# Performance work log

Measured on AMD Instinct MI355X. Metric: run time of the kernel, lower is better.

Reference implementation:

```python
import jax, jax.numpy as jnp
import numpy as np

N_NODES = 50000
N_EDGES = 800000
IN_CH = 64
HID = 128
OUT_AGE, OUT_SEX, OUT_ETH = 21, 2, 5


def _glorot(key, shape):
    fan_in, fan_out = shape
    lim = float(np.sqrt(6.0 / (fan_in + fan_out)))
    return jax.random.uniform(key, shape, jnp.float32, -lim, lim)


def sage_conv(x, src, dst, Wl, Wr, b, n_nodes):
    # PyG SAGEConv (mean aggr): out = lin_l(mean_{j->i} x_j) + lin_r(x_i) + bias
    msg_sum = jax.ops.segment_sum(x[src], dst, num_segments=n_nodes)  # [N, d]
    deg = jax.ops.segment_sum(jnp.ones((src.shape[0],), x.dtype), dst,
                              num_segments=n_nodes)  # [N]
    mean = msg_sum / jnp.maximum(deg, 1.0)[:, None]
    return mean @ Wl + x @ Wr + b


def setup_inputs() -> dict:
    key = jax.random.key(0)
    ks = jax.random.split(key, 16)
    x = jax.random.normal(ks[0], (N_NODES, IN_CH), jnp.float32)
    edge_src = jax.random.randint(ks[1], (N_EDGES,), 0, N_NODES)
    edge_dst = jax.random.randint(ks[2], (N_EDGES,), 0, N_NODES)
    dims = [(IN_CH, HID), (HID, HID), (HID, HID),
            (HID, OUT_AGE), (HID, OUT_SEX), (HID, OUT_ETH)]
    names = ['1', '2', '3', 'age', 'sex', 'eth']
    inp = {'x': x, 'edge_src': edge_src, 'edge_dst': edge_dst}
    for i, (nm, (di, do)) in enumerate(zip(names, dims)):
        inp[f'Wl_{nm}'] = _glorot(ks[3 + 2 * i], (di, do))
        inp[f'Wr_{nm}'] = _glorot(ks[4 + 2 * i], (di, do))
        inp[f'b_{nm}'] = jnp.zeros((do,), jnp.float32)
    return inp


def reference(x, edge_src, edge_dst,
              Wl_1, Wr_1, b_1, Wl_2, Wr_2, b_2, Wl_3, Wr_3, b_3,
              Wl_age, Wr_age, b_age, Wl_sex, Wr_sex, b_sex,
              Wl_eth, Wr_eth, b_eth):
    n = x.shape[0]
    h = jax.nn.relu(sage_conv(x, edge_src, edge_dst, Wl_1, Wr_1, b_1, n))
    h = jax.nn.relu(sage_conv(h, edge_src, edge_dst, Wl_2, Wr_2, b_2, n))
    h = jax.nn.relu(sage_conv(h, edge_src, edge_dst, Wl_3, Wr_3, b_3, n))
    age = sage_conv(h, edge_src, edge_dst, Wl_age, Wr_age, b_age, n)
    sex = sage_conv(h, edge_src, edge_dst, Wl_sex, Wr_sex, b_sex, n)
    eth = sage_conv(h, edge_src, edge_dst, Wl_eth, Wr_eth, b_eth, n)
    return (age, sex, eth)
```

## Files before the change

### kernel.cpp

```cpp
#include <hip/hip_runtime.h>
#include <hip/hip_bf16.h>


typedef __attribute__((ext_vector_type(8))) short bf16x8;
typedef __attribute__((ext_vector_type(4))) float f32x4;

#define NBSH 7
#define EPW  4096

__device__ __forceinline__ unsigned short f2b(float f) {
    __hip_bfloat16 h = __float2bfloat16(f);
    return *reinterpret_cast<unsigned short*>(&h);
}
__device__ __forceinline__ float b2f(unsigned short u) {
    __hip_bfloat16 h;
    *reinterpret_cast<unsigned short*>(&h) = u;
    return __bfloat162float(h);
}

__global__ void bucket_hist(const int* __restrict__ dst, int* __restrict__ ghist,
                            int n_edges, int nb) {
    __shared__ int lh[512];
    int tid = threadIdx.x;
    for (int i = tid; i < 512; i += 256) lh[i] = 0;
    __syncthreads();
    int stride = gridDim.x * blockDim.x;
    for (int e = blockIdx.x * blockDim.x + tid; e < n_edges; e += stride)
        atomicAdd(&lh[dst[e] >> NBSH], 1);
    __syncthreads();
    for (int i = tid; i < nb; i += 256)
        if (lh[i]) atomicAdd(&ghist[i], lh[i]);
}

__global__ void scan_buckets(const int* __restrict__ hist, int* __restrict__ base,
                             int* __restrict__ cur, int nb, int n_edges) {
    __shared__ int tmp[512];
    int t = threadIdx.x;
    int v = (t < nb) ? hist[t] : 0;
    tmp[t] = v;
    __syncthreads();
    for (int off = 1; off < 512; off <<= 1) {
        int u = (t >= off) ? tmp[t - off] : 0;
        __syncthreads();
        tmp[t] += u;
        __syncthreads();
    }
    if (t < nb) {
        base[t] = tmp[t] - v;
        cur[t] = tmp[t] - v;
    }
    if (t == 0) base[nb] = n_edges;
}

__global__ __launch_bounds__(512) void bin_edges_lds(
    const int* __restrict__ src, const int* __restrict__ dst,
    int* __restrict__ bkt_cur, uint2* __restrict__ ebuf, int n_edges, int nb) {
    __shared__ int hist[512];
    __shared__ int hbase[513];
    __shared__ int hcur[512];
    __shared__ uint2 sorted[EPW];
    int tid = threadIdx.x;
    int chunk0 = blockIdx.x * EPW;
    int cnt = min(EPW, n_edges - chunk0);
    hist[tid] = 0;
    __syncthreads();
    for (int i = tid; i < cnt; i += 512) atomicAdd(&hist[dst[chunk0 + i] >> NBSH], 1);
    __syncthreads();
    int v = hist[tid];
    hbase[tid] = v;
    __syncthreads();
    for (int off = 1; off < 512; off <<= 1) {
        int u = (tid >= off) ? hbase[tid - off] : 0;
        __syncthreads();
        hbase[tid] += u;
        __syncthreads();
    }
    int excl = hbase[tid] - v;
    __syncthreads();
    hbase[tid] = excl;
    hcur[tid] = excl;
    if (tid == 511) hbase[512] = excl + v;
    __syncthreads();
    for (int i = tid; i < cnt; i += 512) {
        int s = src[chunk0 + i];
        int d = dst[chunk0 + i];
        int p = atomicAdd(&hcur[d >> NBSH], 1);
        sorted[p] = make_uint2((unsigned)s, (unsigned)d);
    }
    __syncthreads();
    int cntb = hbase[tid + 1] - hbase[tid];
    int gb = 0;
    if (tid < nb && cntb > 0) gb = atomicAdd(&bkt_cur[tid], cntb);
    hist[tid] = gb;
    __syncthreads();
    for (int i = tid; i < cnt; i += 512) {
        uint2 ed = sorted[i];
        int b = (int)(ed.y >> NBSH);
        ebuf[hist[b] + (i - hbase[b])] = ed;
    }
}

__global__ void bucket_degi(const uint2* __restrict__ ebuf, const int* __restrict__ bkt_base,
                            int* __restrict__ degi, int n_nodes) {
    __shared__ int ld[128];
    int b = blockIdx.x, tid = threadIdx.x;
    int lo = b << NBSH;
    if (tid < 128) ld[tid] = 0;
    __syncthreads();
    int s = bkt_base[b], t = bkt_base[b + 1];
    for (int i = s + tid; i < t; i += 256) atomicAdd(&ld[(int)ebuf[i].y - lo], 1);
    __syncthreads();
    int hi = min(lo + 128, n_nodes);
    if (tid < hi - lo) degi[lo + tid] = ld[tid];
}

__global__ void scan_local(const int* __restrict__ degi, int* __restrict__ loc,
                           int* __restrict__ bsum, int n) {
    __shared__ int tmp[256];
    int i = blockIdx.x * 256 + threadIdx.x;
    int v = (i < n) ? degi[i] : 0;
    tmp[threadIdx.x] = v;
    __syncthreads();
    for (int off = 1; off < 256; off <<= 1) {
        int t = (threadIdx.x >= off) ? tmp[threadIdx.x - off] : 0;
        __syncthreads();
        tmp[threadIdx.x] += t;
        __syncthreads();
    }
    if (i < n) loc[i] = tmp[threadIdx.x] - v;
    if (threadIdx.x == 255) bsum[blockIdx.x] = tmp[255];
}

__global__ void scan_block(int* __restrict__ bsum, int nblk) {
    __shared__ int tmp[256];
    int v = (threadIdx.x < nblk) ? bsum[threadIdx.x] : 0;
    tmp[threadIdx.x] = v;
    __syncthreads();
    for (int off = 1; off < 256; off <<= 1) {
        int t = (threadIdx.x >= off) ? tmp[threadIdx.x - off] : 0;
        __syncthreads();
        tmp[threadIdx.x] += t;
        __syncthreads();
    }
    if (threadIdx.x < nblk) bsum[threadIdx.x] = tmp[threadIdx.x] - v;
}

__global__ void scan_add(const int* __restrict__ loc, const int* __restrict__ bsum,
                         int* __restrict__ row_start, int n, int n_edges) {
    int i = blockIdx.x * 256 + threadIdx.x;
    if (i < n) row_start[i] = loc[i] + bsum[blockIdx.x];
    if (i == 0) row_start[n] = n_edges;
}

__global__ void scatter2(const uint2* __restrict__ ebuf, const int* __restrict__ bkt_base,
                         const int* __restrict__ row_start, int* __restrict__ col,
                         int n_nodes) {
    __shared__ int lcur[128];
    int b = blockIdx.x, tid = threadIdx.x;
    int lo = b << NBSH;
    int hi = min(lo + 128, n_nodes);
    if (tid < hi - lo) lcur[tid] = row_start[lo + tid];
    __syncthreads();
    int s = bkt_base[b], t = bkt_base[b + 1];
    for (int i = s + tid; i < t; i += 256) {
        uint2 ed = ebuf[i];
        int p = atomicAdd(&lcur[(int)ed.y - lo], 1);
        col[p] = (int)ed.x;
    }
}

__global__ void convert_x(const float* __restrict__ x, unsigned short* __restrict__ xb,
                          int n4) {
    int t = blockIdx.x * blockDim.x + threadIdx.x;
    if (t >= n4) return;
    float4 v = reinterpret_cast<const float4*>(x)[t];
    uint2 o;
    o.x = (unsigned)f2b(v.x) | ((unsigned)f2b(v.y) << 16);
    o.y = (unsigned)f2b(v.z) | ((unsigned)f2b(v.w) << 16);
    reinterpret_cast<uint2*>(xb)[t] = o;
}

__global__ void build_bt(const float* __restrict__ Wl, const float* __restrict__ Wr,
                         unsigned short* __restrict__ Bt, int KA) {
    int KTOT = 2 * KA;
    int idx = blockIdx.x * blockDim.x + threadIdx.x;
    if (idx >= 128 * KTOT) return;
    int n = idx / KTOT, k = idx % KTOT;
    float v = (k < KA) ? Wl[k * 128 + n] : Wr[(k - KA) * 128 + n];
    Bt[idx] = f2b(v);
}

__global__ void cat_kernel(const float* __restrict__ Wl_age, const float* __restrict__ Wl_sex,
                           const float* __restrict__ Wl_eth, const float* __restrict__ Wr_age,
                           const float* __restrict__ Wr_sex, const float* __restrict__ Wr_eth,
                           const float* __restrict__ b_age, const float* __restrict__ b_sex,
                           const float* __restrict__ b_eth, float* __restrict__ Wl_cat,
                           float* __restrict__ Wr_cat, float* __restrict__ b_cat) {
    int idx = blockIdx.x * blockDim.x + threadIdx.x;
    if (idx < 128 * 28) {
        int k = idx / 28, j = idx % 28;
        float vl, vr;
        if (j < 21) {
            vl = Wl_age[k * 21 + j];
            vr = Wr_age[k * 21 + j];
        } else if (j < 23) {
            vl = Wl_sex[k * 2 + (j - 21)];
            vr = Wr_sex[k * 2 + (j - 21)];
        } else {
            vl = Wl_eth[k * 5 + (j - 23)];
            vr = Wr_eth[k * 5 + (j - 23)];
        }
        Wl_cat[idx] = vl;
        Wr_cat[idx] = vr;
    }
    if (idx < 28) {
        b_cat[idx] = (idx < 21) ? b_age[idx] : (idx < 23) ? b_sex[idx - 21] : b_eth[idx - 23];
    }
}

__global__ void agg128_bf(const unsigned short* __restrict__ feat,
                          const int* __restrict__ row_start, const int* __restrict__ col,
                          unsigned short* __restrict__ mean, int n_nodes) {
    int wave = (blockIdx.x * blockDim.x + threadIdx.x) >> 6;
    int lane = threadIdx.x & 63;
    if (wave >= n_nodes) return;
    int s0 = row_start[wave];
    int deg = row_start[wave + 1] - s0;
    const unsigned* f2 = reinterpret_cast<const unsigned*>(feat);
    float a0 = 0.f, a1 = 0.f, b0 = 0.f, b1 = 0.f;
    float c0 = 0.f, c1 = 0.f, d0 = 0.f, d1 = 0.f;
    for (int base = 0; base < deg; base += 64) {
        int blk = min(64, deg - base);
        int cv = col[s0 + base + min(lane, blk - 1)];
        int i = 0;
        for (; i + 3 < blk; i += 4) {
            int e0 = __shfl(cv, i), e1 = __shfl(cv, i + 1);
            int e2 = __shfl(cv, i + 2), e3 = __shfl(cv, i + 3);
            unsigned u0 = f2[(size_t)e0 * 64 + lane];
            unsigned u1 = f2[(size_t)e1 * 64 + lane];
            unsigned u2 = f2[(size_t)e2 * 64 + lane];
            unsigned u3 = f2[(size_t)e3 * 64 + lane];
            a0 += b2f((unsigned short)(u0 & 0xffff)); a1 += b2f((unsigned short)(u0 >> 16));
            b0 += b2f((unsigned short)(u1 & 0xffff)); b1 += b2f((unsigned short)(u1 >> 16));
            c0 += b2f((unsigned short)(u2 & 0xffff)); c1 += b2f((unsigned short)(u2 >> 16));
            d0 += b2f((unsigned short)(u3 & 0xffff)); d1 += b2f((unsigned short)(u3 >> 16));
        }
        for (; i < blk; ++i) {
            int e0 = __shfl(cv, i);
            unsigned u0 = f2[(size_t)e0 * 64 + lane];
            a0 += b2f((unsigned short)(u0 & 0xffff)); a1 += b2f((unsigned short)(u0 >> 16));
        }
    }
    float inv = (deg > 0) ? 1.0f / (float)deg : 0.0f;
    float sA = (a0 + b0) + (c0 + d0);
    float sB = (a1 + b1) + (c1 + d1);
    unsigned o = (unsigned)f2b(sA * inv) | ((unsigned)f2b(sB * inv) << 16);
    reinterpret_cast<unsigned*>(mean)[(size_t)wave * 64 + lane] = o;
}

__global__ void agg64_bf(const unsigned short* __restrict__ feat,
                         const int* __restrict__ row_start, const int* __restrict__ col,
                         unsigned short* __restrict__ mean, int n_nodes) {
    int wave = (blockIdx.x * blockDim.x + threadIdx.x) >> 6;
    int lane = threadIdx.x & 63;
    if (wave >= n_nodes) return;
    int sub = lane >> 5;
    int lp = lane & 31;
    int s0 = row_start[wave];
    int s1 = row_start[wave + 1];
    const unsigned* f2 = reinterpret_cast<const unsigned*>(feat);
    float a0 = 0.f, a1 = 0.f;
    for (int e = s0 + sub; e < s1; e += 2) {
        unsigned u = f2[(size_t)col[e] * 32 + lp];
        a0 += b2f((unsigned short)(u & 0xffff));
        a1 += b2f((unsigned short)(u >> 16));
    }
    a0 += __shfl_down(a0, 32);
    a1 += __shfl_down(a1, 32);
    if (sub == 0) {
        int deg = s1 - s0;
        float inv = (deg > 0) ? 1.0f / (float)deg : 0.0f;
        unsigned o = (unsigned)f2b(a0 * inv) | ((unsigned)f2b(a1 * inv) << 16);
        reinterpret_cast<unsigned*>(mean)[(size_t)wave * 32 + lp] = o;
    }
}

template <int KTOT, int KA>
__global__ __launch_bounds__(256) void mfma_layer(
    const unsigned short* __restrict__ A0, const unsigned short* __restrict__ A1,
    const unsigned short* __restrict__ Bt, const float* __restrict__ bias,
    unsigned short* __restrict__ out, int n_nodes) {
    constexpr int KC = KTOT / 64;
    __shared__ __align__(16) unsigned short sA[64][72];
    __shared__ __align__(16) unsigned short sB[128][72];
    int node0 = blockIdx.x * 64;
    int tid = threadIdx.x;
    int w = tid >> 6, lane = tid & 63;
    f32x4 acc[8] = {};
    for (int kc = 0; kc < KC; ++kc) {
        const unsigned short* Asrc;
        int kbase, aw;
        if (kc * 64 < KA) { Asrc = A0; kbase = kc * 64; aw = KA; }
        else              { Asrc = A1; kbase = kc * 64 - KA; aw = KTOT - KA; }
        {
            int nd = tid >> 2, k16 = (tid & 3) * 16;
            uint4 v0 = {0, 0, 0, 0}, v1 = {0, 0, 0, 0};
            int gn = node0 + nd;
            if (gn < n_nodes) {
                const uint4* src = reinterpret_cast<const uint4*>(Asrc + (size_t)gn * aw + kbase + k16);
                v0 = src[0];
                v1 = src[1];
            }
            uint4* dst = reinterpret_cast<uint4*>(&sA[nd][k16]);
            dst[0] = v0;
            dst[1] = v1;
        }
        {
            int n = tid >> 1, k32 = (tid & 1) * 32;
            const uint4* src = reinterpret_cast<const uint4*>(Bt + (size_t)n * KTOT + kc * 64 + k32);
            uint4* dst = reinterpret_cast<uint4*>(&sB[n][k32]);
            dst[0] = src[0];
            dst[1] = src[1];
            dst[2] = src[2];
            dst[3] = src[3];
        }
        __syncthreads();
#pragma unroll
        for (int ks = 0; ks < 2; ++ks) {
            int kl = ks * 32 + (lane >> 4) * 8;
            bf16x8 af = *reinterpret_cast<const bf16x8*>(&sA[w * 16 + (lane & 15)][kl]);
#pragma unroll
            for (int t = 0; t < 8; ++t) {
                bf16x8 bfr = *reinterpret_cast<const bf16x8*>(&sB[t * 16 + (lane & 15)][kl]);
                acc[t] = __builtin_amdgcn_mfma_f32_16x16x32_bf16(af, bfr, acc[t], 0, 0, 0);
            }
        }
        __syncthreads();
    }
    int r0 = w * 16, cq = lane >> 4, cr = lane & 15;
#pragma unroll
    for (int t = 0; t < 8; ++t) {
        int colj = t * 16 + cr;
        float bv = bias[colj];
#pragma unroll
        for (int i = 0; i < 4; ++i) {
            int node = node0 + r0 + cq * 4 + i;
            if (node < n_nodes) {
                float v = fmaxf(acc[t][i] + bv, 0.0f);
                out[(size_t)node * 128 + colj] = f2b(v);
            }
        }
    }
}

__global__ void proj_kernel(const unsigned short* __restrict__ h,
                            const float* __restrict__ Wl_cat, float* __restrict__ p,
                            int n_nodes) {
    const int NPB = 4;
    int node0 = blockIdx.x * NPB;
    __shared__ float sh[NPB][128];
    for (int idx = threadIdx.x; idx < NPB * 128; idx += blockDim.x) {
        int n = idx >> 7, k = idx & 127;
        int node = node0 + n;
        if (node < n_nodes) sh[n][k] = b2f(h[(size_t)node * 128 + k]);
    }
    __syncthreads();
    int n = threadIdx.x >> 5, j = threadIdx.x & 31;
    int node = node0 + n;
    if (node >= n_nodes) return;
    float acc = 0.f;
    if (j < 28)
        for (int k = 0; k < 128; k++) acc += sh[n][k] * Wl_cat[k * 28 + j];
    p[(size_t)node * 32 + j] = acc;
}

__global__ void agg_gather32(const float* __restrict__ p, const int* __restrict__ row_start,
                             const int* __restrict__ col, float* __restrict__ meanp,
                             int n_nodes) {
    int gid = blockIdx.x * blockDim.x + threadIdx.x;
    int node = gid >> 5;
    int j = gid & 31;
    if (node >= n_nodes) return;
    int s0 = row_start[node];
    int s1 = row_start[node + 1];
    float a = 0.f, b = 0.f;
    int e = s0;
    for (; e + 1 < s1; e += 2) {
        a += p[(size_t)col[e] * 32 + j];
        b += p[(size_t)col[e + 1] * 32 + j];
    }
    if (e < s1) a += p[(size_t)col[e] * 32 + j];
    int deg = s1 - s0;
    float inv = (deg > 0) ? 1.0f / (float)deg : 0.0f;
    meanp[(size_t)node * 32 + j] = (a + b) * inv;
}

__global__ void head_out_kernel(const unsigned short* __restrict__ h,
                                const float* __restrict__ meanp,
                                const float* __restrict__ Wr_cat, const float* __restrict__ b_cat,
                                float* __restrict__ age, float* __restrict__ sex,
                                float* __restrict__ eth, int n_nodes) {
    const int NPB = 4;
    int node0 = blockIdx.x * NPB;
    __shared__ float sh[NPB][128];
    for (int idx = threadIdx.x; idx < NPB * 128; idx += blockDim.x) {
        int n = idx >> 7, k = idx & 127;
        int node = node0 + n;
        if (node < n_nodes) sh[n][k] = b2f(h[(size_t)node * 128 + k]);
    }
    __syncthreads();
    int n = threadIdx.x >> 5, j = threadIdx.x & 31;
    int node = node0 + n;
    if (node >= n_nodes || j >= 28) return;
    float acc = b_cat[j] + meanp[(size_t)node * 32 + j];
    for (int k = 0; k < 128; k++) acc += sh[n][k] * Wr_cat[k * 28 + j];
    if (j < 21)
        age[(size_t)node * 21 + j] = acc;
    else if (j < 23)
        sex[(size_t)node * 2 + (j - 21)] = acc;
    else
        eth[(size_t)node * 5 + (j - 23)] = acc;
}

extern "C" void kernel_launch(void* const* d_in, const int* in_sizes, int n_in,
                              void* d_out, int out_size, void* d_ws, size_t ws_size,
                              hipStream_t stream) {
    const float* x        = (const float*)d_in[0];
    const int*   edge_src = (const int*)d_in[1];
    const int*   edge_dst = (const int*)d_in[2];
    const float* Wl_1 = (const float*)d_in[3];
    const float* Wr_1 = (const float*)d_in[4];
    const float* b_1  = (const float*)d_in[5];
    const float* Wl_2 = (const float*)d_in[6];
    const float* Wr_2 = (const float*)d_in[7];
    const float* b_2  = (const float*)d_in[8];
    const float* Wl_3 = (const float*)d_in[9];
    const float* Wr_3 = (const float*)d_in[10];
    const float* b_3  = (const float*)d_in[11];
    const float* Wl_age = (const float*)d_in[12];
    const float* Wr_age = (const float*)d_in[13];
    const float* b_age  = (const float*)d_in[14];
    const float* Wl_sex = (const float*)d_in[15];
    const float* Wr_sex = (const float*)d_in[16];
    const float* b_sex  = (const float*)d_in[17];
    const float* Wl_eth = (const float*)d_in[18];
    const float* Wr_eth = (const float*)d_in[19];
    const float* b_eth  = (const float*)d_in[20];

    const int n_nodes = in_sizes[0] / 64;
    const int n_edges = in_sizes[1];

    char* ws = (char*)d_ws;
    int*            degi      = (int*)(ws + 0);
    int*            row_start = (int*)(ws + 200192);
    int*            col       = (int*)(ws + 600576);
    unsigned short* Bt1       = (unsigned short*)(ws + 3800832);
    unsigned short* Bt2       = (unsigned short*)(ws + 3833600);
    unsigned short* Bt3       = (unsigned short*)(ws + 3899136);
    float*          Wl_cat    = (float*)(ws + 3964672);
    float*          Wr_cat    = (float*)(ws + 3979008);
    float*          b_cat     = (float*)(ws + 3993344);
    unsigned short* xb        = (unsigned short*)(ws + 3993600);
    unsigned short* h_bf      = (unsigned short*)(ws + 10393856);
    unsigned short* mean_bf   = (unsigned short*)(ws + 23194112);
    float*          p         = (float*)(ws + 35994368);
    float*          meanp     = (float*)(ws + 42394624);
    int*            scan_loc  = (int*)(ws + 48794880);
    int*            scan_bsum = (int*)(ws + 48995072);
    uint2*          ebuf      = (uint2*)p;
    int*            bkt_hist  = (int*)meanp;
    int*            bkt_base  = bkt_hist + 512;
    int*            bkt_cur   = bkt_hist + 1032;

    float* out_age = (float*)d_out;
    float* out_sex = out_age + (size_t)n_nodes * 21;
    float* out_eth = out_sex + (size_t)n_nodes * 2;

    const int nb        = (n_nodes + 127) >> NBSH;
    const int nchunks   = (n_edges + EPW - 1) / EPW;
    const int nblk_scan = (n_nodes + 255) / 256;

    hipMemsetAsync(bkt_hist, 0, 512 * sizeof(int), stream);
    bucket_hist<<<256, 256, 0, stream>>>(edge_dst, bkt_hist, n_edges, nb);
    scan_buckets<<<1, 512, 0, stream>>>(bkt_hist, bkt_base, bkt_cur, nb, n_edges);
    bin_edges_lds<<<nchunks, 512, 0, stream>>>(edge_src, edge_dst, bkt_cur, ebuf, n_edges, nb);
    bucket_degi<<<nb, 256, 0, stream>>>(ebuf, bkt_base, degi, n_nodes);
    scan_local<<<nblk_scan, 256, 0, stream>>>(degi, scan_loc, scan_bsum, n_nodes);
    scan_block<<<1, 256, 0, stream>>>(scan_bsum, nblk_scan);
    scan_add<<<nblk_scan, 256, 0, stream>>>(scan_loc, scan_bsum, row_start, n_nodes, n_edges);
    scatter2<<<nb, 256, 0, stream>>>(ebuf, bkt_base, row_start, col, n_nodes);

    convert_x<<<(n_nodes * 64 / 4 + 255) / 256, 256, 0, stream>>>(x, xb, n_nodes * 64 / 4);
    build_bt<<<(128 * 128 + 255) / 256, 256, 0, stream>>>(Wl_1, Wr_1, Bt1, 64);
    build_bt<<<(128 * 256 + 255) / 256, 256, 0, stream>>>(Wl_2, Wr_2, Bt2, 128);
    build_bt<<<(128 * 256 + 255) / 256, 256, 0, stream>>>(Wl_3, Wr_3, Bt3, 128);
    cat_kernel<<<(128 * 28 + 255) / 256, 256, 0, stream>>>(
        Wl_age, Wl_sex, Wl_eth, Wr_age, Wr_sex, Wr_eth, b_age, b_sex, b_eth,
        Wl_cat, Wr_cat, b_cat);

    const int agg_grid  = (n_nodes * 64 + 255) / 256;
    const int gemm_grid = (n_nodes + 63) / 64;

    agg64_bf<<<agg_grid, 256, 0, stream>>>(xb, row_start, col, mean_bf, n_nodes);
    mfma_layer<128, 64><<<gemm_grid, 256, 0, stream>>>(mean_bf, xb, Bt1, b_1, h_bf, n_nodes);

    agg128_bf<<<agg_grid, 256, 0, stream>>>(h_bf, row_start, col, mean_bf, n_nodes);
    mfma_layer<256, 128><<<gemm_grid, 256, 0, stream>>>(mean_bf, h_bf, Bt2, b_2, h_bf, n_nodes);

    agg128_bf<<<agg_grid, 256, 0, stream>>>(h_bf, row_start, col, mean_bf, n_nodes);
    mfma_layer<256, 128><<<gemm_grid, 256, 0, stream>>>(mean_bf, h_bf, Bt3, b_3, h_bf, n_nodes);

    proj_kernel<<<(n_nodes + 3) / 4, 128, 0, stream>>>(h_bf, Wl_cat, p, n_nodes);
    agg_gather32<<<(n_nodes * 32 + 255) / 256, 256, 0, stream>>>(p, row_start, col, meanp, n_nodes);
    head_out_kernel<<<(n_nodes + 3) / 4, 128, 0, stream>>>(
        h_bf, meanp, Wr_cat, b_cat, out_age, out_sex, out_eth, n_nodes);
}
```

Measured before the change: 391.1 us.

## Fuse prep kernels and batch neighbor index loads in 64/32-wide gathers

Merges the x conversion, the three weight-transpose kernels and the head-weight concatenation into one prep_all launch, removing four kernel launches. agg64_bf and agg_gather32 now load a block of column indices cooperatively, broadcast them with shuffles, and keep four independent accumulators, so more feature loads are in flight at once. The costs are extra shuffle instructions and more registers per thread.

```diff
diff --git a/kernel.cpp b/kernel.cpp
--- a/kernel.cpp
+++ b/kernel.cpp
@@ -169,52 +169,72 @@
     }
 }
 
-__global__ void convert_x(const float* __restrict__ x, unsigned short* __restrict__ xb,
-                          int n4) {
-    int t = blockIdx.x * blockDim.x + threadIdx.x;
-    if (t >= n4) return;
-    float4 v = reinterpret_cast<const float4*>(x)[t];
-    uint2 o;
-    o.x = (unsigned)f2b(v.x) | ((unsigned)f2b(v.y) << 16);
-    o.y = (unsigned)f2b(v.z) | ((unsigned)f2b(v.w) << 16);
-    reinterpret_cast<uint2*>(xb)[t] = o;
-}
-
-__global__ void build_bt(const float* __restrict__ Wl, const float* __restrict__ Wr,
-                         unsigned short* __restrict__ Bt, int KA) {
+__device__ __forceinline__ void bt_body(const float* __restrict__ Wl,
+                                        const float* __restrict__ Wr,
+                                        unsigned short* __restrict__ Bt,
+                                        int KA, int idx) {
     int KTOT = 2 * KA;
-    int idx = blockIdx.x * blockDim.x + threadIdx.x;
     if (idx >= 128 * KTOT) return;
     int n = idx / KTOT, k = idx % KTOT;
     float v = (k < KA) ? Wl[k * 128 + n] : Wr[(k - KA) * 128 + n];
     Bt[idx] = f2b(v);
 }
 
-__global__ void cat_kernel(const float* __restrict__ Wl_age, const float* __restrict__ Wl_sex,
-                           const float* __restrict__ Wl_eth, const float* __restrict__ Wr_age,
-                           const float* __restrict__ Wr_sex, const float* __restrict__ Wr_eth,
-                           const float* __restrict__ b_age, const float* __restrict__ b_sex,
-                           const float* __restrict__ b_eth, float* __restrict__ Wl_cat,
-                           float* __restrict__ Wr_cat, float* __restrict__ b_cat) {
-    int idx = blockIdx.x * blockDim.x + threadIdx.x;
-    if (idx < 128 * 28) {
-        int k = idx / 28, j = idx % 28;
-        float vl, vr;
-        if (j < 21) {
-            vl = Wl_age[k * 21 + j];
-            vr = Wr_age[k * 21 + j];
-        } else if (j < 23) {
-            vl = Wl_sex[k * 2 + (j - 21)];
-            vr = Wr_sex[k * 2 + (j - 21)];
-        } else {
-            vl = Wl_eth[k * 5 + (j - 23)];
-            vr = Wr_eth[k * 5 + (j - 23)];
-        }
-        Wl_cat[idx] = vl;
-        Wr_cat[idx] = vr;
-    }
-    if (idx < 28) {
-        b_cat[idx] = (idx < 21) ? b_age[idx] : (idx < 23) ? b_sex[idx - 21] : b_eth[idx - 23];
+__global__ void prep_all(const float* __restrict__ x, unsigned short* __restrict__ xb, int n4,
+                         const float* __restrict__ Wl1, const float* __restrict__ Wr1,
+                         unsigned short* __restrict__ Bt1,
+                         const float* __restrict__ Wl2, const float* __restrict__ Wr2,
+                         unsigned short* __restrict__ Bt2,
+                         const float* __restrict__ Wl3, const float* __restrict__ Wr3,
+                         unsigned short* __restrict__ Bt3,
+                         const float* __restrict__ Wl_age, const float* __restrict__ Wl_sex,
+                         const float* __restrict__ Wl_eth,
+                         const float* __restrict__ Wr_age, const float* __restrict__ Wr_sex,
+                         const float* __restrict__ Wr_eth,
+                         const float* __restrict__ b_age, const float* __restrict__ b_sex,
+                         const float* __restrict__ b_eth,
+                         float* __restrict__ Wl_cat, float* __restrict__ Wr_cat,
+                         float* __restrict__ b_cat) {
+    int nbx = (n4 + 255) / 256;
+    int b = blockIdx.x;
+    if (b < nbx) {
+        int t = b * 256 + threadIdx.x;
+        if (t < n4) {
+            float4 v = reinterpret_cast<const float4*>(x)[t];
+            uint2 o;
+            o.x = (unsigned)f2b(v.x) | ((unsigned)f2b(v.y) << 16);
+            o.y = (unsigned)f2b(v.z) | ((unsigned)f2b(v.w) << 16);
+            reinterpret_cast<uint2*>(xb)[t] = o;
+        }
+        return;
+    }
+    b -= nbx;
+    if (b < 64)  { bt_body(Wl1, Wr1, Bt1, 64,  b * 256 + threadIdx.x); return; }
+    b -= 64;
+    if (b < 128) { bt_body(Wl2, Wr2, Bt2, 128, b * 256 + threadIdx.x); return; }
+    b -= 128;
+    if (b < 128) { bt_body(Wl3, Wr3, Bt3, 128, b * 256 + threadIdx.x); return; }
+    b -= 128;
+    {
+        int idx = b * 256 + threadIdx.x;
+        if (idx < 128 * 28) {
+            int k = idx / 28, j = idx % 28;
+            float vl, vr;
+            if (j < 21) {
+                vl = Wl_age[k * 21 + j];
+                vr = Wr_age[k * 21 + j];
+            } else if (j < 23) {
+                vl = Wl_sex[k * 2 + (j - 21)];
+                vr = Wr_sex[k * 2 + (j - 21)];
+            } else {
+                vl = Wl_eth[k * 5 + (j - 23)];
+                vr = Wr_eth[k * 5 + (j - 23)];
+            }
+            Wl_cat[idx] = vl;
+            Wr_cat[idx] = vr;
+        }
+        if (idx < 28)
+            b_cat[idx] = (idx < 21) ? b_age[idx] : (idx < 23) ? b_sex[idx - 21] : b_eth[idx - 23];
     }
 }
 
@@ -264,23 +284,44 @@
     int wave = (blockIdx.x * blockDim.x + threadIdx.x) >> 6;
     int lane = threadIdx.x & 63;
     if (wave >= n_nodes) return;
-    int sub = lane >> 5;
+    int half = lane >> 5;
     int lp = lane & 31;
     int s0 = row_start[wave];
-    int s1 = row_start[wave + 1];
+    int deg = row_start[wave + 1] - s0;
     const unsigned* f2 = reinterpret_cast<const unsigned*>(feat);
-    float a0 = 0.f, a1 = 0.f;
-    for (int e = s0 + sub; e < s1; e += 2) {
-        unsigned u = f2[(size_t)col[e] * 32 + lp];
-        a0 += b2f((unsigned short)(u & 0xffff));
-        a1 += b2f((unsigned short)(u >> 16));
-    }
-    a0 += __shfl_down(a0, 32);
-    a1 += __shfl_down(a1, 32);
-    if (sub == 0) {
-        int deg = s1 - s0;
+    float a0 = 0.f, a1 = 0.f, b0 = 0.f, b1 = 0.f;
+    float c0 = 0.f, c1 = 0.f, d0 = 0.f, d1 = 0.f;
+    for (int base = 0; base < deg; base += 64) {
+        int blk = min(64, deg - base);
+        int cv = col[s0 + base + min(lane, blk - 1)];
+        int nfull = blk & ~7;
+        for (int i = half * 4; i < nfull; i += 8) {
+            int e0 = __shfl(cv, i), e1 = __shfl(cv, i + 1);
+            int e2 = __shfl(cv, i + 2), e3 = __shfl(cv, i + 3);
+            unsigned u0 = f2[(size_t)e0 * 32 + lp];
+            unsigned u1 = f2[(size_t)e1 * 32 + lp];
+            unsigned u2 = f2[(size_t)e2 * 32 + lp];
+            unsigned u3 = f2[(size_t)e3 * 32 + lp];
+            a0 += b2f((unsigned short)(u0 & 0xffff)); a1 += b2f((unsigned short)(u0 >> 16));
+            b0 += b2f((unsigned short)(u1 & 0xffff)); b1 += b2f((unsigned short)(u1 >> 16));
+            c0 += b2f((unsigned short)(u2 & 0xffff)); c1 += b2f((unsigned short)(u2 >> 16));
+            d0 += b2f((unsigned short)(u3 & 0xffff)); d1 += b2f((unsigned short)(u3 >> 16));
+        }
+        int tstart = nfull + half * 4;
+        int tend = min(blk, tstart + 4);
+        for (int i = tstart; i < tend; ++i) {
+            int e0 = __shfl(cv, i);
+            unsigned u0 = f2[(size_t)e0 * 32 + lp];
+            a0 += b2f((unsigned short)(u0 & 0xffff)); a1 += b2f((unsigned short)(u0 >> 16));
+        }
+    }
+    float sA = (a0 + b0) + (c0 + d0);
+    float sB = (a1 + b1) + (c1 + d1);
+    sA += __shfl_down(sA, 32);
+    sB += __shfl_down(sB, 32);
+    if (half == 0) {
         float inv = (deg > 0) ? 1.0f / (float)deg : 0.0f;
-        unsigned o = (unsigned)f2b(a0 * inv) | ((unsigned)f2b(a1 * inv) << 16);
+        unsigned o = (unsigned)f2b(sA * inv) | ((unsigned)f2b(sB * inv) << 16);
         reinterpret_cast<unsigned*>(mean)[(size_t)wave * 32 + lp] = o;
     }
 }
@@ -377,22 +418,33 @@
 __global__ void agg_gather32(const float* __restrict__ p, const int* __restrict__ row_start,
                              const int* __restrict__ col, float* __restrict__ meanp,
                              int n_nodes) {
-    int gid = blockIdx.x * blockDim.x + threadIdx.x;
-    int node = gid >> 5;
-    int j = gid & 31;
+    int node = (blockIdx.x * blockDim.x + threadIdx.x) >> 5;
+    int lane = threadIdx.x & 63;
+    int lp = lane & 31;
+    int grpbase = lane & 32;
     if (node >= n_nodes) return;
     int s0 = row_start[node];
-    int s1 = row_start[node + 1];
-    float a = 0.f, b = 0.f;
-    int e = s0;
-    for (; e + 1 < s1; e += 2) {
-        a += p[(size_t)col[e] * 32 + j];
-        b += p[(size_t)col[e + 1] * 32 + j];
-    }
-    if (e < s1) a += p[(size_t)col[e] * 32 + j];
-    int deg = s1 - s0;
+    int deg = row_start[node + 1] - s0;
+    float a = 0.f, b = 0.f, c = 0.f, d = 0.f;
+    for (int base = 0; base < deg; base += 32) {
+        int blk = min(32, deg - base);
+        int cv = col[s0 + base + min(lp, blk - 1)];
+        int i = 0;
+        for (; i + 3 < blk; i += 4) {
+            int e0 = __shfl(cv, grpbase + i),     e1 = __shfl(cv, grpbase + i + 1);
+            int e2 = __shfl(cv, grpbase + i + 2), e3 = __shfl(cv, grpbase + i + 3);
+            a += p[(size_t)e0 * 32 + lp];
+            b += p[(size_t)e1 * 32 + lp];
+            c += p[(size_t)e2 * 32 + lp];
+            d += p[(size_t)e3 * 32 + lp];
+        }
+        for (; i < blk; ++i) {
+            int e0 = __shfl(cv, grpbase + i);
+            a += p[(size_t)e0 * 32 + lp];
+        }
+    }
     float inv = (deg > 0) ? 1.0f / (float)deg : 0.0f;
-    meanp[(size_t)node * 32 + j] = (a + b) * inv;
+    meanp[(size_t)node * 32 + lp] = ((a + b) + (c + d)) * inv;
 }
 
 __global__ void head_out_kernel(const unsigned short* __restrict__ h,
@@ -479,6 +531,7 @@
     const int nb        = (n_nodes + 127) >> NBSH;
     const int nchunks   = (n_edges + EPW - 1) / EPW;
     const int nblk_scan = (n_nodes + 255) / 256;
+    const int n4        = n_nodes * 64 / 4;
 
     hipMemsetAsync(bkt_hist, 0, 512 * sizeof(int), stream);
     bucket_hist<<<256, 256, 0, stream>>>(edge_dst, bkt_hist, n_edges, nb);
@@ -490,13 +543,13 @@
     scan_add<<<nblk_scan, 256, 0, stream>>>(scan_loc, scan_bsum, row_start, n_nodes, n_edges);
     scatter2<<<nb, 256, 0, stream>>>(ebuf, bkt_base, row_start, col, n_nodes);
 
-    convert_x<<<(n_nodes * 64 / 4 + 255) / 256, 256, 0, stream>>>(x, xb, n_nodes * 64 / 4);
-    build_bt<<<(128 * 128 + 255) / 256, 256, 0, stream>>>(Wl_1, Wr_1, Bt1, 64);
-    build_bt<<<(128 * 256 + 255) / 256, 256, 0, stream>>>(Wl_2, Wr_2, Bt2, 128);
-    build_bt<<<(128 * 256 + 255) / 256, 256, 0, stream>>>(Wl_3, Wr_3, Bt3, 128);
-    cat_kernel<<<(128 * 28 + 255) / 256, 256, 0, stream>>>(
-        Wl_age, Wl_sex, Wl_eth, Wr_age, Wr_sex, Wr_eth, b_age, b_sex, b_eth,
-        Wl_cat, Wr_cat, b_cat);
+    {
+        int grid = (n4 + 255) / 256 + 64 + 128 + 128 + 14;
+        prep_all<<<grid, 256, 0, stream>>>(
+            x, xb, n4, Wl_1, Wr_1, Bt1, Wl_2, Wr_2, Bt2, Wl_3, Wr_3, Bt3,
+            Wl_age, Wl_sex, Wl_eth, Wr_age, Wr_sex, Wr_eth, b_age, b_sex, b_eth,
+            Wl_cat, Wr_cat, b_cat);
+    }
 
     const int agg_grid  = (n_nodes * 64 + 255) / 256;
     const int gemm_grid = (n_nodes + 63) / 64;
```

Measured after the change: 348.5 us. 10.9% less time.
